# Optimization experiments

Measured on AMD Instinct MI355X. Metric: run time of the kernel, lower is better.

Reference implementation:

```python
import jax, jax.numpy as jnp
import numpy as np

TD = 256  # text_dim


def conv1x1(x, w, b):
    # 1x1 conv == per-pixel matmul over channels; w: [out,in], x: [B,C,H,W]
    return jnp.einsum('oc,bchw->bohw', w, x) + b[None, :, None, None]


def setup_inputs() -> dict:
    key = jax.random.key(0)
    ks = iter(jax.random.split(key, 48))
    B = 4
    cin = [64, 128, 256, 512]
    vshapes = [(B, 64, 64, 64), (B, 128, 32, 32), (B, 256, 16, 16), (B, 512, 8, 8)]
    tshapes = [(B, TD, 64, 64), (B, TD, 32, 32), (B, TD, 16, 16), (B, TD, 8, 8)]
    d = {}
    for i, s in enumerate(vshapes):
        d[f'v{i}'] = jax.random.normal(next(ks), s, jnp.float32)
    for i, s in enumerate(tshapes):
        d[f't{i}'] = jax.random.normal(next(ks), s, jnp.float32)
    for i in range(4):
        d[f'vp_w{i}'] = jax.random.normal(next(ks), (TD, cin[i]), jnp.float32) / np.float32(np.sqrt(cin[i]))
        d[f'vp_b{i}'] = jnp.zeros((TD,), jnp.float32)
        d[f'op_w{i}'] = jax.random.normal(next(ks), (cin[i], TD), jnp.float32) / np.float32(np.sqrt(TD))
        d[f'op_b{i}'] = jnp.zeros((cin[i],), jnp.float32)
    for nm in ['q', 'k', 'v']:
        d[f'{nm}_w'] = jax.random.normal(next(ks), (TD, TD), jnp.float32) / np.float32(np.sqrt(TD))
        d[f'{nm}_b'] = jnp.zeros((TD,), jnp.float32)
    d['sg_w'] = jax.random.normal(next(ks), (TD, 4 * TD), jnp.float32) / np.float32(np.sqrt(4 * TD))
    d['sg_b'] = jnp.zeros((TD,), jnp.float32)
    d['bn_g'] = jnp.ones((TD,), jnp.float32)
    d['bn_b'] = jnp.zeros((TD,), jnp.float32)
    d['fc1_w'] = jax.random.normal(next(ks), (1024, TD), jnp.float32) / np.float32(np.sqrt(TD))
    d['fc1_b'] = jnp.zeros((1024,), jnp.float32)
    d['fc2_w'] = jax.random.normal(next(ks), (2048, 1024), jnp.float32) / np.float32(np.sqrt(1024))
    d['fc2_b'] = jnp.zeros((2048,), jnp.float32)
    return d


def reference(v0, v1, v2, v3, t0, t1, t2, t3,
              vp_w0, vp_b0, op_w0, op_b0,
              vp_w1, vp_b1, op_w1, op_b1,
              vp_w2, vp_b2, op_w2, op_b2,
              vp_w3, vp_b3, op_w3, op_b3,
              q_w, q_b, k_w, k_b, v_w, v_b,
              sg_w, sg_b, bn_g, bn_b, fc1_w, fc1_b, fc2_w, fc2_b):
    vs = [v0, v1, v2, v3]
    ts = [t0, t1, t2, t3]
    vpw = [vp_w0, vp_w1, vp_w2, vp_w3]
    vpb = [vp_b0, vp_b1, vp_b2, vp_b3]
    opw = [op_w0, op_w1, op_w2, op_w3]
    opb = [op_b0, op_b1, op_b2, op_b3]
    scale = np.float32(1.0 / np.sqrt(TD))

    enhanced = []
    for i in range(4):
        vp = conv1x1(vs[i], vpw[i], vpb[i])          # [B,TD,H,W]
        q = conv1x1(vp, q_w, q_b)
        k = conv1x1(ts[i], k_w, k_b)
        v = conv1x1(ts[i], v_w, v_b)
        B, C, H, W = vp.shape
        qf = q.reshape(B, C, H * W)                  # [B,C,Nq]
        kf = k.reshape(B, C, -1)                     # [B,C,Nk]
        vf = v.reshape(B, C, -1)                     # [B,C,Nk]
        attn = jax.nn.softmax(jnp.einsum('bcn,bcm->bnm', qf, kf) * scale, axis=-1)  # [B,Nq,Nk]
        av = jnp.einsum('bcm,bnm->bcn', vf, attn).reshape(B, C, H, W)
        enhanced.append(conv1x1(av, opw[i], opb[i]) + vs[i])

    # align text maps to smallest spatial size (divisible -> block average pool)
    s = ts[3].shape[2]
    pooled = [t.reshape(t.shape[0], t.shape[1], s, t.shape[2] // s, s, t.shape[3] // s).mean(axis=(3, 5))
              for t in ts]
    cat = jnp.concatenate(pooled, axis=1)            # [B,4*TD,s,s]
    x = conv1x1(cat, sg_w, sg_b)                     # [B,TD,s,s]
    # BatchNorm2d, training mode (batch statistics, biased variance)
    mu = x.mean(axis=(0, 2, 3), keepdims=True)
    var = x.var(axis=(0, 2, 3), keepdims=True)
    x = (x - mu) * jax.lax.rsqrt(var + 1e-5) * bn_g[None, :, None, None] + bn_b[None, :, None, None]
    x = jax.nn.relu(x).mean(axis=(2, 3))             # global avg pool -> [B,TD]
    x = jax.nn.relu(x @ fc1_w.T + fc1_b)
    x = x @ fc2_w.T + fc2_b                          # [B,2048]
    semantic = x.reshape(-1, 2, 1024)
    return (semantic, enhanced[0], enhanced[1], enhanced[2], enhanced[3])
```

## Files before the change

kernel.cpp:

```cpp
#include <hip/hip_runtime.h>

typedef __bf16 bf16_t;
typedef bf16_t bf16x8 __attribute__((ext_vector_type(8)));
typedef float f32x4 __attribute__((ext_vector_type(4)));
typedef unsigned short u16;
typedef unsigned long long u64;

__device__ __forceinline__ u16 f2bf(float f) {
  union { float f; unsigned u; } v; v.f = f;
  unsigned r = v.u + 0x7FFFu + ((v.u >> 16) & 1u);
  return (u16)(r >> 16);
}
__device__ __forceinline__ bf16x8 ld8(const u16* p) {
  return *reinterpret_cast<const bf16x8*>(p);
}
__device__ __forceinline__ void gload_lds16(const void* g, void* l) {
  __builtin_amdgcn_global_load_lds(
      (const __attribute__((address_space(1))) void*)g,
      (__attribute__((address_space(3))) void*)l, 16, 0, 0);
}

struct Ptrs4 { const float* p[4]; };

struct CvtJob { const float* s; u16* d; int n; };
struct CvtJobs { CvtJob j[8]; };

__global__ __launch_bounds__(256) void cvt_multi(CvtJobs jobs) {
  CvtJob J = jobs.j[blockIdx.y];
  for (int i = blockIdx.x * 256 + threadIdx.x; i < J.n; i += gridDim.x * 256)
    J.d[i] = f2bf(J.s[i]);
}

struct TJob { const float* s; u16* d; int C, N, nbx, nbz, off; };
struct TJobs { TJob j[12]; };

__global__ __launch_bounds__(256) void transpose_batch(TJobs J, int nj) {
  int bid = blockIdx.x, ji = 0;
#pragma unroll
  for (int k = 1; k < 12; ++k)
    if (k < nj && bid >= J.j[k].off) ji = k;
  TJob job = J.j[ji];
  int local = bid - job.off;
  int z = local % job.nbz;
  int l2 = local / job.nbz;
  int bx = l2 % job.nbx, by = l2 / job.nbx;
  __shared__ float t[32][33];
  int tx = threadIdx.x & 31, ty = threadIdx.x >> 5;
  int n0 = bx * 32, c0 = by * 32;
  long zi = (long)z * job.C * job.N, zo = (long)z * job.N * job.C;
#pragma unroll
  for (int i = 0; i < 4; ++i)
    t[ty + 8 * i][tx] = job.s[zi + (long)(c0 + ty + 8 * i) * job.N + n0 + tx];
  __syncthreads();
#pragma unroll
  for (int i = 0; i < 4; ++i)
    job.d[zo + (long)(n0 + ty + 8 * i) * job.C + c0 + tx] = f2bf(t[tx][ty + 8 * i]);
}

struct GJob {
  const u16 *A, *X;
  const float *bias, *bias2;
  void *o1, *o2;
  const float* res;
  int M, N, K, nbx, nbz, off;
};
struct GJobs { GJob j[5]; };

template <int MODE>
__global__ __launch_bounds__(256) void gemm_batch(GJobs J, int nj) {
  int bid = blockIdx.x, ji = 0;
#pragma unroll
  for (int k = 1; k < 5; ++k)
    if (k < nj && bid >= J.j[k].off) ji = k;
  GJob job = J.j[ji];
  int local = bid - job.off;
  const int z = local % job.nbz;
  int l2 = local / job.nbz;
  const int n0 = (l2 % job.nbx) * 64, m0 = (l2 / job.nbx) * 64;
  const int M = job.M, N = job.N, K = job.K;
  const u16* __restrict__ A = job.A;
  const u16* __restrict__ X = job.X;

  __shared__ __attribute__((aligned(16))) u16 As[64][40];
  __shared__ __attribute__((aligned(16))) u16 Bs[64][40];
  const int tid = threadIdx.x;
  const long Xz = (long)z * N * K;
  const int arow = tid >> 2, acol = (tid & 3) * 8;
  const int w = tid >> 6, lane = tid & 63, g = lane >> 4, ln = lane & 15;
  const int wm = (w >> 1) * 32, wn = (w & 1) * 32;
  f32x4 zero = {0.f, 0.f, 0.f, 0.f};
  f32x4 acc[2][2];
#pragma unroll
  for (int i = 0; i < 2; ++i)
#pragma unroll
    for (int j = 0; j < 2; ++j) acc[i][j] = zero;

  for (int k0 = 0; k0 < K; k0 += 32) {
    int4 av = *reinterpret_cast<const int4*>(A + (long)(m0 + arow) * K + k0 + acol);
    int4 bv = *reinterpret_cast<const int4*>(X + Xz + (long)(n0 + arow) * K + k0 + acol);
    __syncthreads();
    *reinterpret_cast<int4*>(&As[arow][acol]) = av;
    *reinterpret_cast<int4*>(&Bs[arow][acol]) = bv;
    __syncthreads();
    bf16x8 a0 = ld8(&As[wm + ln][g * 8]);
    bf16x8 a1 = ld8(&As[wm + 16 + ln][g * 8]);
    bf16x8 b0 = ld8(&Bs[wn + ln][g * 8]);
    bf16x8 b1 = ld8(&Bs[wn + 16 + ln][g * 8]);
    acc[0][0] = __builtin_amdgcn_mfma_f32_16x16x32_bf16(a0, b0, acc[0][0], 0, 0, 0);
    acc[0][1] = __builtin_amdgcn_mfma_f32_16x16x32_bf16(a0, b1, acc[0][1], 0, 0, 0);
    acc[1][0] = __builtin_amdgcn_mfma_f32_16x16x32_bf16(a1, b0, acc[1][0], 0, 0, 0);
    acc[1][1] = __builtin_amdgcn_mfma_f32_16x16x32_bf16(a1, b1, acc[1][1], 0, 0, 0);
  }

#pragma unroll
  for (int i = 0; i < 2; ++i) {
#pragma unroll
    for (int j = 0; j < 2; ++j) {
      int mr0 = m0 + wm + 16 * i + g * 4;
      int nc = n0 + wn + 16 * j + ln;
      if (MODE == 0) {
        u64 pk = 0;
#pragma unroll
        for (int r = 0; r < 4; ++r) {
          float val = acc[i][j][r] + (job.bias ? job.bias[mr0 + r] : 0.f);
          pk |= (u64)f2bf(val) << (16 * r);
        }
        *reinterpret_cast<u64*>((u16*)job.o1 + ((long)z * N + nc) * M + mr0) = pk;
      } else if (MODE == 1) {
#pragma unroll
        for (int r = 0; r < 4; ++r) {
          float val = acc[i][j][r] + (job.bias ? job.bias[mr0 + r] : 0.f);
          ((u16*)job.o1)[((long)z * M + mr0 + r) * N + nc] = f2bf(val);
        }
      } else if (MODE == 2) {
#pragma unroll
        for (int r = 0; r < 4; ++r) {
          long idx = ((long)z * M + mr0 + r) * N + nc;
          float val = acc[i][j][r] + job.bias[mr0 + r];
          if (job.res) val += job.res[idx];
          ((float*)job.o1)[idx] = val;
        }
      } else {
        long tbase = (long)z * N * 256 + (long)(nc >> 5) * 8192;
        if (mr0 < 256) {
          u64 pk = 0;
#pragma unroll
          for (int r = 0; r < 4; ++r)
            pk |= (u64)f2bf(acc[i][j][r] + job.bias[mr0 + r]) << (16 * r);
          int byteoff = ((nc & 31) * 512 + mr0 * 2) ^ ((nc & 7) << 4);
          *reinterpret_cast<u64*>((char*)job.o1 + tbase * 2 + byteoff) = pk;
        } else {
          int d0 = mr0 - 256;
#pragma unroll
          for (int r = 0; r < 4; ++r)
            ((u16*)job.o2)[tbase + (long)(d0 + r) * 32 + (nc & 31)] =
                f2bf(acc[i][j][r] + job.bias2[d0 + r]);
        }
      }
    }
  }
}

struct AJob { const u16 *Q, *K, *V; u16* O; int N, off; };
struct AJobs { AJob j[4]; };

__global__ __launch_bounds__(256, 2) void attn_batch(AJobs J, int nj) {
  __shared__ __attribute__((aligned(16))) char stK[2][2][16384];
  __shared__ __attribute__((aligned(16))) u16 Ps[4][32][40];
  __shared__ float mls[2][2][2][16];
  int bid = blockIdx.x, ji = 0;
#pragma unroll
  for (int k = 1; k < 4; ++k)
    if (k < nj && bid >= J.j[k].off) ji = k;
  AJob job = J.j[ji];
  int local = bid - job.off;
  const int z = local & 3, bx = local >> 2;
  const int N = job.N;
  const int tid = threadIdx.x;
  const int w = tid >> 6, lane = tid & 63;
  const int g = lane >> 4, ln = lane & 15;
  const int qg = w & 1, kseg = w >> 1;
  const int qbase = bx * 64 + qg * 32;
  const float scale = 0.0625f;
  const int nt = N >> 6;
  const long tb = (long)z * (N >> 5) + (long)kseg * nt;

  bf16x8 qf[2][8];
#pragma unroll
  for (int qh = 0; qh < 2; ++qh) {
    const u16* qp = job.Q + ((long)z * N + qbase + qh * 16 + ln) * 256 + g * 8;
#pragma unroll
    for (int cc = 0; cc < 8; ++cc) qf[qh][cc] = ld8(qp + cc * 32);
  }
  f32x4 zero = {0.f, 0.f, 0.f, 0.f};
  f32x4 oacc[16][2];
#pragma unroll
  for (int ct = 0; ct < 16; ++ct) {
    oacc[ct][0] = zero;
    oacc[ct][1] = zero;
  }
  float mrow[2] = {-1e30f, -1e30f}, lrow[2] = {0.f, 0.f};

  auto stage_K = [&](int buf, int t) {
    const char* gp = (const char*)job.K + (tb + t) * 16384 + qg * 8192 + lane * 16;
    char* lp = &stK[buf][kseg][qg * 8192];
#pragma unroll
    for (int q = 0; q < 8; ++q) gload_lds16(gp + q * 1024, lp + q * 1024);
  };

  stage_K(0, 0);
  asm volatile("s_waitcnt vmcnt(0)" ::: "memory");
  __syncthreads();

  const int swz = (ln & 7) << 4;
  for (int t = 0; t < nt; ++t) {
    const int buf = t & 1;
    if (t + 1 < nt) stage_K(buf ^ 1, t + 1);
    const char* Kb = &stK[buf][kseg][0];
    const u16* Vg = job.V + (tb + t) * 8192;

    f32x4 s[2][2];
    s[0][0] = zero; s[0][1] = zero; s[1][0] = zero; s[1][1] = zero;
#pragma unroll
    for (int cc = 0; cc < 8; ++cc) {
      bf16x8 k0 = *reinterpret_cast<const bf16x8*>(Kb + ((ln * 512 + cc * 64 + g * 16) ^ swz));
      bf16x8 k1 = *reinterpret_cast<const bf16x8*>(Kb + (((16 + ln) * 512 + cc * 64 + g * 16) ^ swz));
      s[0][0] = __builtin_amdgcn_mfma_f32_16x16x32_bf16(k0, qf[0][cc], s[0][0], 0, 0, 0);
      s[0][1] = __builtin_amdgcn_mfma_f32_16x16x32_bf16(k0, qf[1][cc], s[0][1], 0, 0, 0);
      s[1][0] = __builtin_amdgcn_mfma_f32_16x16x32_bf16(k1, qf[0][cc], s[1][0], 0, 0, 0);
      s[1][1] = __builtin_amdgcn_mfma_f32_16x16x32_bf16(k1, qf[1][cc], s[1][1], 0, 0, 0);
    }
    bf16x8 vv[8];
#pragma unroll
    for (int ct = 0; ct < 8; ++ct) vv[ct] = ld8(Vg + (ct * 16 + ln) * 32 + g * 8);

#pragma unroll
    for (int qh = 0; qh < 2; ++qh) {
      float x[8];
#pragma unroll
      for (int r = 0; r < 4; ++r) { x[r] = s[0][qh][r] * scale; x[4 + r] = s[1][qh][r] * scale; }
      float lm = fmaxf(fmaxf(fmaxf(x[0], x[1]), fmaxf(x[2], x[3])),
                       fmaxf(fmaxf(x[4], x[5]), fmaxf(x[6], x[7])));
      lm = fmaxf(lm, __shfl_xor(lm, 16));
      lm = fmaxf(lm, __shfl_xor(lm, 32));
      if (!__all(lm - mrow[qh] <= 8.0f)) {
        float nm = fmaxf(mrow[qh], lm);
        float fac = __expf(mrow[qh] - nm);
        mrow[qh] = nm;
        lrow[qh] *= fac;
#pragma unroll
        for (int ct = 0; ct < 16; ++ct)
#pragma unroll
          for (int r = 0; r < 4; ++r) oacc[ct][qh][r] *= fac;
      }
      float ps = 0.f;
#pragma unroll
      for (int j2 = 0; j2 < 8; ++j2) { x[j2] = __expf(x[j2] - mrow[qh]); ps += x[j2]; }
      ps += __shfl_xor(ps, 16);
      ps += __shfl_xor(ps, 32);
      lrow[qh] += ps;
      u64 plo = (u64)f2bf(x[0]) | ((u64)f2bf(x[1]) << 16) |
                ((u64)f2bf(x[2]) << 32) | ((u64)f2bf(x[3]) << 48);
      u64 phi = (u64)f2bf(x[4]) | ((u64)f2bf(x[5]) << 16) |
                ((u64)f2bf(x[6]) << 32) | ((u64)f2bf(x[7]) << 48);
      *reinterpret_cast<u64*>(&Ps[w][qh * 16 + ln][g * 4]) = plo;
      *reinterpret_cast<u64*>(&Ps[w][qh * 16 + ln][16 + g * 4]) = phi;
    }
    asm volatile("s_waitcnt lgkmcnt(0)" ::: "memory");
    bf16x8 pa0 = ld8(&Ps[w][ln][g * 8]);
    bf16x8 pa1 = ld8(&Ps[w][16 + ln][g * 8]);
#pragma unroll
    for (int ct = 0; ct < 8; ++ct) {
      oacc[ct][0] = __builtin_amdgcn_mfma_f32_16x16x32_bf16(vv[ct], pa0, oacc[ct][0], 0, 0, 0);
      oacc[ct][1] = __builtin_amdgcn_mfma_f32_16x16x32_bf16(vv[ct], pa1, oacc[ct][1], 0, 0, 0);
    }
#pragma unroll
    for (int ct = 0; ct < 8; ++ct) vv[ct] = ld8(Vg + ((ct + 8) * 16 + ln) * 32 + g * 8);
#pragma unroll
    for (int ct = 0; ct < 8; ++ct) {
      oacc[ct + 8][0] = __builtin_amdgcn_mfma_f32_16x16x32_bf16(vv[ct], pa0, oacc[ct + 8][0], 0, 0, 0);
      oacc[ct + 8][1] = __builtin_amdgcn_mfma_f32_16x16x32_bf16(vv[ct], pa1, oacc[ct + 8][1], 0, 0, 0);
    }
    asm volatile("s_waitcnt vmcnt(0)" ::: "memory");
    __syncthreads();
  }

  float* osc = (float*)&stK[0][0][0];
  if (kseg == 1) {
    if (g == 0) {
#pragma unroll
      for (int qh = 0; qh < 2; ++qh) {
        mls[qg][qh][0][ln] = mrow[qh];
        mls[qg][qh][1][ln] = lrow[qh];
      }
    }
#pragma unroll
    for (int ct = 0; ct < 16; ++ct)
#pragma unroll
      for (int qh = 0; qh < 2; ++qh)
#pragma unroll
        for (int r = 0; r < 4; ++r)
          osc[qg * 8192 + (ct * 16 + g * 4 + r) * 32 + qh * 16 + ln] = oacc[ct][qh][r];
  }
  __syncthreads();
  if (kseg == 0) {
    float wa[2], wb[2], rl[2];
#pragma unroll
    for (int qh = 0; qh < 2; ++qh) {
      float mb = mls[qg][qh][0][ln], lb = mls[qg][qh][1][ln];
      float M = fmaxf(mrow[qh], mb);
      wa[qh] = __expf(mrow[qh] - M);
      wb[qh] = __expf(mb - M);
      rl[qh] = 1.f / (wa[qh] * lrow[qh] + wb[qh] * lb);
    }
#pragma unroll
    for (int ct = 0; ct < 16; ++ct)
#pragma unroll
      for (int qh = 0; qh < 2; ++qh) {
        u64 pk = 0;
#pragma unroll
        for (int r = 0; r < 4; ++r) {
          float val = (wa[qh] * oacc[ct][qh][r] +
                       wb[qh] * osc[qg * 8192 + (ct * 16 + g * 4 + r) * 32 + qh * 16 + ln]) *
                      rl[qh];
          pk |= (u64)f2bf(val) << (16 * r);
        }
        *reinterpret_cast<u64*>(job.O + ((long)z * N + qbase + qh * 16 + ln) * 256 +
                                ct * 16 + g * 4) = pk;
      }
  }
}

__global__ __launch_bounds__(256) void qeb_k(const float* __restrict__ qw,
                                             const float* __restrict__ qb, Ptrs4 vpb,
                                             float* __restrict__ qeb) {
  int o = threadIdx.x;
  int lvl = blockIdx.x;
  const float* vb = vpb.p[lvl];
  float acc = qb[o];
  for (int k = 0; k < 256; ++k) acc += qw[o * 256 + k] * vb[k];
  qeb[lvl * 256 + o] = acc;
}

__global__ __launch_bounds__(256) void pool_k(Ptrs4 ts, u16* __restrict__ poolT) {
  int gt = blockIdx.x * 256 + threadIdx.x;
  int ch = gt & 1023;
  int pix = (gt >> 10) & 63;
  int b = gt >> 16;
  int level = ch >> 8, c = ch & 255;
  int H = 64 >> level;
  int f = H >> 3;
  int py = pix >> 3, px = pix & 7;
  const float* src = ts.p[level] + (((long)b * 256 + c) * H + py * f) * H + px * f;
  float s = 0.f;
  for (int dy = 0; dy < f; ++dy)
    for (int dx = 0; dx < f; ++dx) s += src[dy * H + dx];
  poolT[gt] = f2bf(s / (float)(f * f));
}

__global__ __launch_bounds__(64) void bn_k(const float* __restrict__ x,
                                           const float* __restrict__ gw,
                                           const float* __restrict__ gb,
                                           float* __restrict__ xp) {
  int ch = blockIdx.x, t = threadIdx.x;
  float v[4], s = 0.f, sq = 0.f;
#pragma unroll
  for (int b = 0; b < 4; ++b) {
    v[b] = x[((long)b * 256 + ch) * 64 + t];
    s += v[b];
    sq += v[b] * v[b];
  }
#pragma unroll
  for (int off = 32; off; off >>= 1) {
    s += __shfl_xor(s, off);
    sq += __shfl_xor(sq, off);
  }
  float mu = s * (1.f / 256.f);
  float var = sq * (1.f / 256.f) - mu * mu;
  float rstd = rsqrtf(var + 1e-5f);
  float G = gw[ch], Bb = gb[ch];
#pragma unroll
  for (int b = 0; b < 4; ++b) {
    float y = fmaxf((v[b] - mu) * rstd * G + Bb, 0.f);
#pragma unroll
    for (int off = 32; off; off >>= 1) y += __shfl_xor(y, off);
    if (t == 0) xp[b * 256 + ch] = y * (1.f / 64.f);
  }
}

__global__ __launch_bounds__(256) void fc1_k(const float* __restrict__ xp,
                                             const float* __restrict__ w,
                                             const float* __restrict__ bias,
                                             float* __restrict__ o1) {
  int gt = blockIdx.x * 256 + threadIdx.x;
  int b = gt >> 10, j = gt & 1023;
  float acc = bias[j];
  const float* wr = w + (long)j * 256;
  const float* xr = xp + b * 256;
  for (int k = 0; k < 256; ++k) acc += xr[k] * wr[k];
  o1[gt] = fmaxf(acc, 0.f);
}

__global__ __launch_bounds__(256) void fc2_k(const float* __restrict__ o1,
                                             const float* __restrict__ w,
                                             const float* __restrict__ bias,
                                             float* __restrict__ out) {
  int gt = blockIdx.x * 256 + threadIdx.x;
  int b = gt >> 11, o = gt & 2047;
  float acc = bias[o];
  const float* wr = w + (long)o * 1024;
  const float* xr = o1 + b * 1024;
  for (int k = 0; k < 1024; ++k) acc += xr[k] * wr[k];
  out[gt] = acc;
}

extern "C" void kernel_launch(void* const* d_in, const int* in_sizes, int n_in,
                              void* d_out, int out_size, void* d_ws, size_t ws_size,
                              hipStream_t stream) {
  (void)in_sizes; (void)n_in; (void)out_size; (void)ws_size;
  const float *v_in[4], *t_in[4], *vp_w[4], *vp_b[4], *op_w[4], *op_b[4];
  for (int i = 0; i < 4; ++i) {
    v_in[i] = (const float*)d_in[i];
    t_in[i] = (const float*)d_in[4 + i];
    vp_w[i] = (const float*)d_in[8 + 4 * i];
    vp_b[i] = (const float*)d_in[9 + 4 * i];
    op_w[i] = (const float*)d_in[10 + 4 * i];
    op_b[i] = (const float*)d_in[11 + 4 * i];
  }
  const float* q_w = (const float*)d_in[24];
  const float* q_b = (const float*)d_in[25];
  const float* k_w = (const float*)d_in[26];
  const float* k_b = (const float*)d_in[27];
  const float* v_w = (const float*)d_in[28];
  const float* v_b = (const float*)d_in[29];
  const float* sg_w = (const float*)d_in[30];
  const float* sg_b = (const float*)d_in[31];
  const float* bn_g = (const float*)d_in[32];
  const float* bn_b = (const float*)d_in[33];
  const float* fc1_w = (const float*)d_in[34];
  const float* fc1_b = (const float*)d_in[35];
  const float* fc2_w = (const float*)d_in[36];
  const float* fc2_b = (const float*)d_in[37];
  float* out = (float*)d_out;

  const int cin[4] = {64, 128, 256, 512};
  const int NN[4] = {4096, 1024, 256, 64};
  const long NOFF[4] = {0, 4194304, 5242880, 5505024};
  const long VOFF[4] = {0, 1048576, 1572864, 1835008};

  char* ws = (char*)d_ws;
  size_t off = 0;
  auto alloc = [&](size_t bytes) {
    void* p = ws + off;
    off += (bytes + 255) & ~(size_t)255;
    return p;
  };
  u16* w_q = (u16*)alloc(65536 * 2);
  u16* w_kv = (u16*)alloc(131072 * 2);
  u16* w_op[4];
  for (int i = 0; i < 4; ++i) w_op[i] = (u16*)alloc((size_t)cin[i] * 256 * 2);
  u16* w_sg = (u16*)alloc(262144 * 2);
  u16* vpwT[4];
  for (int i = 0; i < 4; ++i) vpwT[i] = (u16*)alloc((size_t)cin[i] * 256 * 2);
  u16* qe[4];
  for (int i = 0; i < 4; ++i) qe[i] = (u16*)alloc((size_t)256 * cin[i] * 2);
  float* qeb = (float*)alloc(1024 * 4);
  u16* vT = (u16*)alloc((size_t)1966080 * 2);
  u16* tT = (u16*)alloc((size_t)5570560 * 2);
  u16* QT = (u16*)alloc((size_t)5570560 * 2);
  u16* Kt = (u16*)alloc((size_t)5570560 * 2);
  u16* Vt = (u16*)alloc((size_t)5570560 * 2);
  u16* Ob = (u16*)alloc((size_t)5570560 * 2);
  u16* poolT = (u16*)alloc((size_t)262144 * 2);
  float* xbuf = (float*)alloc((size_t)65536 * 4);
  float* xp = (float*)alloc(1024 * 4);
  float* fc1o = (float*)alloc(4096 * 4);

  CvtJobs jobs;
  jobs.j[0] = {q_w, w_q, 65536};
  jobs.j[1] = {k_w, w_kv, 65536};
  jobs.j[2] = {v_w, w_kv + 65536, 65536};
  jobs.j[3] = {op_w[0], w_op[0], cin[0] * 256};
  jobs.j[4] = {op_w[1], w_op[1], cin[1] * 256};
  jobs.j[5] = {op_w[2], w_op[2], cin[2] * 256};
  jobs.j[6] = {op_w[3], w_op[3], cin[3] * 256};
  jobs.j[7] = {sg_w, w_sg, 262144};
  cvt_multi<<<dim3(32, 8), 256, 0, stream>>>(jobs);

  {
    TJobs T;
    int boff = 0, nj = 0;
    for (int i = 0; i < 4; ++i) {
      int nbx = cin[i] / 32;
      T.j[nj] = {vp_w[i], vpwT[i], 256, cin[i], nbx, 1, boff};
      boff += nbx * 8;
      ++nj;
    }
    for (int i = 0; i < 4; ++i) {
      int nbx = NN[i] / 32, nby = cin[i] / 32;
      T.j[nj] = {v_in[i], vT + VOFF[i], cin[i], NN[i], nbx, 4, boff};
      boff += nbx * nby * 4;
      ++nj;
    }
    for (int i = 0; i < 4; ++i) {
      int nbx = NN[i] / 32;
      T.j[nj] = {t_in[i], tT + NOFF[i], 256, NN[i], nbx, 4, boff};
      boff += nbx * 8 * 4;
      ++nj;
    }
    transpose_batch<<<boff, 256, 0, stream>>>(T, nj);
  }

  {
    GJobs G;
    int boff = 0;
    for (int i = 0; i < 4; ++i) {
      int nbx = cin[i] / 64;
      G.j[i] = {w_q, vpwT[i], nullptr, nullptr, qe[i], nullptr, nullptr,
                256, cin[i], 256, nbx, 1, boff};
      boff += nbx * 4;
    }
    gemm_batch<1><<<boff, 256, 0, stream>>>(G, 4);
  }
  Ptrs4 vpbp;
  for (int i = 0; i < 4; ++i) vpbp.p[i] = vp_b[i];
  qeb_k<<<4, 256, 0, stream>>>(q_w, q_b, vpbp, qeb);

  {
    GJobs G;
    int boff = 0;
    for (int i = 0; i < 4; ++i) {
      int nbx = NN[i] / 64;
      G.j[i] = {qe[i], vT + VOFF[i], qeb + 256 * i, nullptr, QT + NOFF[i], nullptr,
                nullptr, 256, NN[i], cin[i], nbx, 4, boff};
      boff += nbx * 4 * 4;
    }
    gemm_batch<0><<<boff, 256, 0, stream>>>(G, 4);
  }

  {
    GJobs G;
    int boff = 0;
    for (int i = 0; i < 4; ++i) {
      int nbx = NN[i] / 64;
      G.j[i] = {w_kv, tT + NOFF[i], k_b, v_b, Kt + NOFF[i], Vt + NOFF[i], nullptr,
                512, NN[i], 256, nbx, 4, boff};
      boff += nbx * 8 * 4;
    }
    gemm_batch<3><<<boff, 256, 0, stream>>>(G, 4);
  }

  {
    AJobs A;
    int boff = 0;
    for (int i = 0; i < 4; ++i) {
      A.j[i] = {QT + NOFF[i], Kt + NOFF[i], Vt + NOFF[i], Ob + NOFF[i], NN[i], boff};
      boff += (NN[i] / 64) * 4;
    }
    attn_batch<<<boff, 256, 0, stream>>>(A, 4);
  }

  Ptrs4 tp;
  for (int i = 0; i < 4; ++i) tp.p[i] = t_in[i];
  pool_k<<<1024, 256, 0, stream>>>(tp, poolT);

  const long enh_off[4] = {8192, 8192 + 1048576, 8192 + 1048576 + 524288,
                           8192 + 1048576 + 524288 + 262144};
  {
    GJobs G;
    int boff = 0;
    for (int i = 0; i < 4; ++i) {
      int nbx = NN[i] / 64, nby = cin[i] / 64;
      G.j[i] = {w_op[i], Ob + NOFF[i], op_b[i], nullptr, out + enh_off[i], nullptr,
                v_in[i], cin[i], NN[i], 256, nbx, 4, boff};
      boff += nbx * nby * 4;
    }
    G.j[4] = {w_sg, poolT, sg_b, nullptr, xbuf, nullptr, nullptr,
              256, 64, 1024, 1, 4, boff};
    boff += 1 * 4 * 4;
    gemm_batch<2><<<boff, 256, 0, stream>>>(G, 5);
  }

  bn_k<<<256, 64, 0, stream>>>(xbuf, bn_g, bn_b, xp);
  fc1_k<<<16, 256, 0, stream>>>(xp, fc1_w, fc1_b, fc1o);
  fc2_k<<<32, 256, 0, stream>>>(fc1o, fc2_w, fc2_b, out);
}
```

Baseline: 458.4 us.

## Stage V tiles in swizzled LDS and merge Q and KV projection launches

The attention kernel now has each wave own 16 query rows and walk the whole key range. It drops the split-K scheme and its cross-wave merge through shared memory. K and V tiles of 32 keys are both staged into LDS asynchronously, so V is no longer read straight from global memory. To support this, the V output of the KV projection is written in a swizzled layout. The Q projection and KV projection GEMMs are fused into one launch by making the epilogue mode a runtime field, which adds branch overhead in the epilogue.

Result: faster. 378.7 us (-17.4%).

```diff
diff --git a/kernel.cpp b/kernel.cpp
--- a/kernel.cpp
+++ b/kernel.cpp
@@ -62,15 +62,14 @@
   const float *bias, *bias2;
   void *o1, *o2;
   const float* res;
-  int M, N, K, nbx, nbz, off;
+  int M, N, K, nbx, nbz, off, mode;
 };
-struct GJobs { GJob j[5]; };
-
-template <int MODE>
+struct GJobs { GJob j[8]; };
+
 __global__ __launch_bounds__(256) void gemm_batch(GJobs J, int nj) {
   int bid = blockIdx.x, ji = 0;
 #pragma unroll
-  for (int k = 1; k < 5; ++k)
+  for (int k = 1; k < 8; ++k)
     if (k < nj && bid >= J.j[k].off) ji = k;
   GJob job = J.j[ji];
   int local = bid - job.off;
@@ -118,7 +117,7 @@
     for (int j = 0; j < 2; ++j) {
       int mr0 = m0 + wm + 16 * i + g * 4;
       int nc = n0 + wn + 16 * j + ln;
-      if (MODE == 0) {
+      if (job.mode == 0) {
         u64 pk = 0;
 #pragma unroll
         for (int r = 0; r < 4; ++r) {
@@ -126,13 +125,13 @@
           pk |= (u64)f2bf(val) << (16 * r);
         }
         *reinterpret_cast<u64*>((u16*)job.o1 + ((long)z * N + nc) * M + mr0) = pk;
-      } else if (MODE == 1) {
+      } else if (job.mode == 1) {
 #pragma unroll
         for (int r = 0; r < 4; ++r) {
           float val = acc[i][j][r] + (job.bias ? job.bias[mr0 + r] : 0.f);
           ((u16*)job.o1)[((long)z * M + mr0 + r) * N + nc] = f2bf(val);
         }
-      } else if (MODE == 2) {
+      } else if (job.mode == 2) {
 #pragma unroll
         for (int r = 0; r < 4; ++r) {
           long idx = ((long)z * M + mr0 + r) * N + nc;
@@ -152,9 +151,12 @@
         } else {
           int d0 = mr0 - 256;
 #pragma unroll
-          for (int r = 0; r < 4; ++r)
-            ((u16*)job.o2)[tbase + (long)(d0 + r) * 32 + (nc & 31)] =
-                f2bf(acc[i][j][r] + job.bias2[d0 + r]);
+          for (int r = 0; r < 4; ++r) {
+            int d = d0 + r;
+            int byteoff = (d * 64 + (nc & 31) * 2) ^ ((d & 7) << 4);
+            *reinterpret_cast<u16*>((char*)job.o2 + tbase * 2 + byteoff) =
+                f2bf(acc[i][j][r] + job.bias2[d]);
+          }
         }
       }
     }
@@ -165,9 +167,8 @@
 struct AJobs { AJob j[4]; };
 
 __global__ __launch_bounds__(256, 2) void attn_batch(AJobs J, int nj) {
-  __shared__ __attribute__((aligned(16))) char stK[2][2][16384];
-  __shared__ __attribute__((aligned(16))) u16 Ps[4][32][40];
-  __shared__ float mls[2][2][2][16];
+  __shared__ __attribute__((aligned(16))) char stKV[2][2][16384];
+  __shared__ __attribute__((aligned(16))) u16 Ps[4][16][40];
   int bid = blockIdx.x, ji = 0;
 #pragma unroll
   for (int k = 1; k < 4; ++k)
@@ -179,155 +180,99 @@
   const int tid = threadIdx.x;
   const int w = tid >> 6, lane = tid & 63;
   const int g = lane >> 4, ln = lane & 15;
-  const int qg = w & 1, kseg = w >> 1;
-  const int qbase = bx * 64 + qg * 32;
+  const int qrow = bx * 64 + w * 16 + ln;
   const float scale = 0.0625f;
-  const int nt = N >> 6;
-  const long tb = (long)z * (N >> 5) + (long)kseg * nt;
-
-  bf16x8 qf[2][8];
-#pragma unroll
-  for (int qh = 0; qh < 2; ++qh) {
-    const u16* qp = job.Q + ((long)z * N + qbase + qh * 16 + ln) * 256 + g * 8;
-#pragma unroll
-    for (int cc = 0; cc < 8; ++cc) qf[qh][cc] = ld8(qp + cc * 32);
+  const int nt = N >> 5;
+  const long tb = (long)z * nt;
+
+  bf16x8 qf[8];
+  {
+    const u16* qp = job.Q + ((long)z * N + qrow) * 256 + g * 8;
+#pragma unroll
+    for (int cc = 0; cc < 8; ++cc) qf[cc] = ld8(qp + cc * 32);
   }
   f32x4 zero = {0.f, 0.f, 0.f, 0.f};
-  f32x4 oacc[16][2];
-#pragma unroll
-  for (int ct = 0; ct < 16; ++ct) {
-    oacc[ct][0] = zero;
-    oacc[ct][1] = zero;
-  }
-  float mrow[2] = {-1e30f, -1e30f}, lrow[2] = {0.f, 0.f};
-
-  auto stage_K = [&](int buf, int t) {
-    const char* gp = (const char*)job.K + (tb + t) * 16384 + qg * 8192 + lane * 16;
-    char* lp = &stK[buf][kseg][qg * 8192];
+  f32x4 oacc[16];
+#pragma unroll
+  for (int ct = 0; ct < 16; ++ct) oacc[ct] = zero;
+  float mrow = -1e30f, lrow = 0.f;
+
+  const char* gsrc = (const char*)(w < 2 ? job.K : job.V);
+  auto stage_tile = [&](int buf, int t) {
+    const char* gp = gsrc + (tb + t) * 16384 + (w & 1) * 8192 + lane * 16;
+    char* lp = &stKV[buf][w >> 1][(w & 1) * 8192];
 #pragma unroll
     for (int q = 0; q < 8; ++q) gload_lds16(gp + q * 1024, lp + q * 1024);
   };
 
-  stage_K(0, 0);
+  stage_tile(0, 0);
   asm volatile("s_waitcnt vmcnt(0)" ::: "memory");
   __syncthreads();
 
   const int swz = (ln & 7) << 4;
   for (int t = 0; t < nt; ++t) {
     const int buf = t & 1;
-    if (t + 1 < nt) stage_K(buf ^ 1, t + 1);
-    const char* Kb = &stK[buf][kseg][0];
-    const u16* Vg = job.V + (tb + t) * 8192;
-
-    f32x4 s[2][2];
-    s[0][0] = zero; s[0][1] = zero; s[1][0] = zero; s[1][1] = zero;
+    if (t + 1 < nt) stage_tile(buf ^ 1, t + 1);
+    const char* Kb = &stKV[buf][0][0];
+    const char* Vb = &stKV[buf][1][0];
+
+    f32x4 s0 = zero, s1 = zero;
 #pragma unroll
     for (int cc = 0; cc < 8; ++cc) {
       bf16x8 k0 = *reinterpret_cast<const bf16x8*>(Kb + ((ln * 512 + cc * 64 + g * 16) ^ swz));
       bf16x8 k1 = *reinterpret_cast<const bf16x8*>(Kb + (((16 + ln) * 512 + cc * 64 + g * 16) ^ swz));
-      s[0][0] = __builtin_amdgcn_mfma_f32_16x16x32_bf16(k0, qf[0][cc], s[0][0], 0, 0, 0);
-      s[0][1] = __builtin_amdgcn_mfma_f32_16x16x32_bf16(k0, qf[1][cc], s[0][1], 0, 0, 0);
-      s[1][0] = __builtin_amdgcn_mfma_f32_16x16x32_bf16(k1, qf[0][cc], s[1][0], 0, 0, 0);
-      s[1][1] = __builtin_amdgcn_mfma_f32_16x16x32_bf16(k1, qf[1][cc], s[1][1], 0, 0, 0);
-    }
-    bf16x8 vv[8];
-#pragma unroll
-    for (int ct = 0; ct < 8; ++ct) vv[ct] = ld8(Vg + (ct * 16 + ln) * 32 + g * 8);
-
-#pragma unroll
-    for (int qh = 0; qh < 2; ++qh) {
-      float x[8];
-#pragma unroll
-      for (int r = 0; r < 4; ++r) { x[r] = s[0][qh][r] * scale; x[4 + r] = s[1][qh][r] * scale; }
-      float lm = fmaxf(fmaxf(fmaxf(x[0], x[1]), fmaxf(x[2], x[3])),
-                       fmaxf(fmaxf(x[4], x[5]), fmaxf(x[6], x[7])));
-      lm = fmaxf(lm, __shfl_xor(lm, 16));
-      lm = fmaxf(lm, __shfl_xor(lm, 32));
-      if (!__all(lm - mrow[qh] <= 8.0f)) {
-        float nm = fmaxf(mrow[qh], lm);
-        float fac = __expf(mrow[qh] - nm);
-        mrow[qh] = nm;
-        lrow[qh] *= fac;
-#pragma unroll
-        for (int ct = 0; ct < 16; ++ct)
-#pragma unroll
-          for (int r = 0; r < 4; ++r) oacc[ct][qh][r] *= fac;
-      }
-      float ps = 0.f;
-#pragma unroll
-      for (int j2 = 0; j2 < 8; ++j2) { x[j2] = __expf(x[j2] - mrow[qh]); ps += x[j2]; }
-      ps += __shfl_xor(ps, 16);
-      ps += __shfl_xor(ps, 32);
-      lrow[qh] += ps;
-      u64 plo = (u64)f2bf(x[0]) | ((u64)f2bf(x[1]) << 16) |
-                ((u64)f2bf(x[2]) << 32) | ((u64)f2bf(x[3]) << 48);
-      u64 phi = (u64)f2bf(x[4]) | ((u64)f2bf(x[5]) << 16) |
-                ((u64)f2bf(x[6]) << 32) | ((u64)f2bf(x[7]) << 48);
-      *reinterpret_cast<u64*>(&Ps[w][qh * 16 + ln][g * 4]) = plo;
-      *reinterpret_cast<u64*>(&Ps[w][qh * 16 + ln][16 + g * 4]) = phi;
-    }
+      s0 = __builtin_amdgcn_mfma_f32_16x16x32_bf16(k0, qf[cc], s0, 0, 0, 0);
+      s1 = __builtin_amdgcn_mfma_f32_16x16x32_bf16(k1, qf[cc], s1, 0, 0, 0);
+    }
+    float x[8];
+#pragma unroll
+    for (int r = 0; r < 4; ++r) { x[r] = s0[r] * scale; x[4 + r] = s1[r] * scale; }
+    float lm = fmaxf(fmaxf(fmaxf(x[0], x[1]), fmaxf(x[2], x[3])),
+                     fmaxf(fmaxf(x[4], x[5]), fmaxf(x[6], x[7])));
+    lm = fmaxf(lm, __shfl_xor(lm, 16));
+    lm = fmaxf(lm, __shfl_xor(lm, 32));
+    if (!__all(lm - mrow <= 8.0f)) {
+      float nm = fmaxf(mrow, lm);
+      float fac = __expf(mrow - nm);
+      mrow = nm;
+      lrow *= fac;
+#pragma unroll
+      for (int ct = 0; ct < 16; ++ct)
+#pragma unroll
+        for (int r = 0; r < 4; ++r) oacc[ct][r] *= fac;
+    }
+    float ps = 0.f;
+#pragma unroll
+    for (int j2 = 0; j2 < 8; ++j2) { x[j2] = __expf(x[j2] - mrow); ps += x[j2]; }
+    ps += __shfl_xor(ps, 16);
+    ps += __shfl_xor(ps, 32);
+    lrow += ps;
+    u64 plo = (u64)f2bf(x[0]) | ((u64)f2bf(x[1]) << 16) |
+              ((u64)f2bf(x[2]) << 32) | ((u64)f2bf(x[3]) << 48);
+    u64 phi = (u64)f2bf(x[4]) | ((u64)f2bf(x[5]) << 16) |
+              ((u64)f2bf(x[6]) << 32) | ((u64)f2bf(x[7]) << 48);
+    *reinterpret_cast<u64*>(&Ps[w][ln][g * 4]) = plo;
+    *reinterpret_cast<u64*>(&Ps[w][ln][16 + g * 4]) = phi;
     asm volatile("s_waitcnt lgkmcnt(0)" ::: "memory");
-    bf16x8 pa0 = ld8(&Ps[w][ln][g * 8]);
-    bf16x8 pa1 = ld8(&Ps[w][16 + ln][g * 8]);
-#pragma unroll
-    for (int ct = 0; ct < 8; ++ct) {
-      oacc[ct][0] = __builtin_amdgcn_mfma_f32_16x16x32_bf16(vv[ct], pa0, oacc[ct][0], 0, 0, 0);
-      oacc[ct][1] = __builtin_amdgcn_mfma_f32_16x16x32_bf16(vv[ct], pa1, oacc[ct][1], 0, 0, 0);
-    }
-#pragma unroll
-    for (int ct = 0; ct < 8; ++ct) vv[ct] = ld8(Vg + ((ct + 8) * 16 + ln) * 32 + g * 8);
-#pragma unroll
-    for (int ct = 0; ct < 8; ++ct) {
-      oacc[ct + 8][0] = __builtin_amdgcn_mfma_f32_16x16x32_bf16(vv[ct], pa0, oacc[ct + 8][0], 0, 0, 0);
-      oacc[ct + 8][1] = __builtin_amdgcn_mfma_f32_16x16x32_bf16(vv[ct], pa1, oacc[ct + 8][1], 0, 0, 0);
+    bf16x8 pa = ld8(&Ps[w][ln][g * 8]);
+#pragma unroll
+    for (int ct = 0; ct < 16; ++ct) {
+      bf16x8 vv = *reinterpret_cast<const bf16x8*>(
+          Vb + (((ct * 16 + ln) * 64 + g * 16) ^ swz));
+      oacc[ct] = __builtin_amdgcn_mfma_f32_16x16x32_bf16(vv, pa, oacc[ct], 0, 0, 0);
     }
     asm volatile("s_waitcnt vmcnt(0)" ::: "memory");
     __syncthreads();
   }
 
-  float* osc = (float*)&stK[0][0][0];
-  if (kseg == 1) {
-    if (g == 0) {
-#pragma unroll
-      for (int qh = 0; qh < 2; ++qh) {
-        mls[qg][qh][0][ln] = mrow[qh];
-        mls[qg][qh][1][ln] = lrow[qh];
-      }
-    }
-#pragma unroll
-    for (int ct = 0; ct < 16; ++ct)
-#pragma unroll
-      for (int qh = 0; qh < 2; ++qh)
-#pragma unroll
-        for (int r = 0; r < 4; ++r)
-          osc[qg * 8192 + (ct * 16 + g * 4 + r) * 32 + qh * 16 + ln] = oacc[ct][qh][r];
-  }
-  __syncthreads();
-  if (kseg == 0) {
-    float wa[2], wb[2], rl[2];
-#pragma unroll
-    for (int qh = 0; qh < 2; ++qh) {
-      float mb = mls[qg][qh][0][ln], lb = mls[qg][qh][1][ln];
-      float M = fmaxf(mrow[qh], mb);
-      wa[qh] = __expf(mrow[qh] - M);
-      wb[qh] = __expf(mb - M);
-      rl[qh] = 1.f / (wa[qh] * lrow[qh] + wb[qh] * lb);
-    }
-#pragma unroll
-    for (int ct = 0; ct < 16; ++ct)
-#pragma unroll
-      for (int qh = 0; qh < 2; ++qh) {
-        u64 pk = 0;
-#pragma unroll
-        for (int r = 0; r < 4; ++r) {
-          float val = (wa[qh] * oacc[ct][qh][r] +
-                       wb[qh] * osc[qg * 8192 + (ct * 16 + g * 4 + r) * 32 + qh * 16 + ln]) *
-                      rl[qh];
-          pk |= (u64)f2bf(val) << (16 * r);
-        }
-        *reinterpret_cast<u64*>(job.O + ((long)z * N + qbase + qh * 16 + ln) * 256 +
-                                ct * 16 + g * 4) = pk;
-      }
+  const float rl = 1.f / lrow;
+  u16* Oz = job.O + ((long)z * N + qrow) * 256;
+#pragma unroll
+  for (int ct = 0; ct < 16; ++ct) {
+    u64 pk = 0;
+#pragma unroll
+    for (int r = 0; r < 4; ++r) pk |= (u64)f2bf(oacc[ct][r] * rl) << (16 * r);
+    *reinterpret_cast<u64*>(Oz + ct * 16 + g * 4) = pk;
   }
 }
 
@@ -517,10 +462,10 @@
     for (int i = 0; i < 4; ++i) {
       int nbx = cin[i] / 64;
       G.j[i] = {w_q, vpwT[i], nullptr, nullptr, qe[i], nullptr, nullptr,
-                256, cin[i], 256, nbx, 1, boff};
+                256, cin[i], 256, nbx, 1, boff, 1};
       boff += nbx * 4;
     }
-    gemm_batch<1><<<boff, 256, 0, stream>>>(G, 4);
+    gemm_batch<<<boff, 256, 0, stream>>>(G, 4);
   }
   Ptrs4 vpbp;
   for (int i = 0; i < 4; ++i) vpbp.p[i] = vp_b[i];
@@ -528,26 +473,22 @@
 
   {
     GJobs G;
-    int boff = 0;
+    int boff = 0, nj = 0;
     for (int i = 0; i < 4; ++i) {
       int nbx = NN[i] / 64;
-      G.j[i] = {qe[i], vT + VOFF[i], qeb + 256 * i, nullptr, QT + NOFF[i], nullptr,
-                nullptr, 256, NN[i], cin[i], nbx, 4, boff};
+      G.j[nj] = {qe[i], vT + VOFF[i], qeb + 256 * i, nullptr, QT + NOFF[i], nullptr,
+                 nullptr, 256, NN[i], cin[i], nbx, 4, boff, 0};
       boff += nbx * 4 * 4;
-    }
-    gemm_batch<0><<<boff, 256, 0, stream>>>(G, 4);
-  }
-
-  {
-    GJobs G;
-    int boff = 0;
+      ++nj;
+    }
     for (int i = 0; i < 4; ++i) {
       int nbx = NN[i] / 64;
-      G.j[i] = {w_kv, tT + NOFF[i], k_b, v_b, Kt + NOFF[i], Vt + NOFF[i], nullptr,
-                512, NN[i], 256, nbx, 4, boff};
+      G.j[nj] = {w_kv, tT + NOFF[i], k_b, v_b, Kt + NOFF[i], Vt + NOFF[i], nullptr,
+                 512, NN[i], 256, nbx, 4, boff, 3};
       boff += nbx * 8 * 4;
-    }
-    gemm_batch<3><<<boff, 256, 0, stream>>>(G, 4);
+      ++nj;
+    }
+    gemm_batch<<<boff, 256, 0, stream>>>(G, 8);
   }
 
   {
@@ -572,13 +513,13 @@
     for (int i = 0; i < 4; ++i) {
       int nbx = NN[i] / 64, nby = cin[i] / 64;
       G.j[i] = {w_op[i], Ob + NOFF[i], op_b[i], nullptr, out + enh_off[i], nullptr,
-                v_in[i], cin[i], NN[i], 256, nbx, 4, boff};
+                v_in[i], cin[i], NN[i], 256, nbx, 4, boff, 2};
       boff += nbx * nby * 4;
     }
     G.j[4] = {w_sg, poolT, sg_b, nullptr, xbuf, nullptr, nullptr,
-              256, 64, 1024, 1, 4, boff};
+              256, 64, 1024, 1, 4, boff, 2};
     boff += 1 * 4 * 4;
-    gemm_batch<2><<<boff, 256, 0, stream>>>(G, 5);
+    gemm_batch<<<boff, 256, 0, stream>>>(G, 5);
   }
 
   bn_k<<<256, 64, 0, stream>>>(xbuf, bn_g, bn_b, xp);
```
